# Optimization experiments

Measured on AMD Instinct MI355X. Metric: run time of the kernel, lower is better.

Reference implementation:

```python
import jax, jax.numpy as jnp
import numpy as np

DEPTH = 13                 # tree depth -> N = 2**DEPTH - 1 reaches (heap layout, outlet = node 0)
N = 2 ** DEPTH - 1         # 8191 reaches
T = 2048                   # timesteps


def setup_inputs() -> dict:
    key = jax.random.key(0)
    ks = jax.random.split(key, 8)
    u = lambda k, shape, lo, hi: jax.random.uniform(k, shape, minval=lo, maxval=hi, dtype=jnp.float32)
    return {
        "lateral_inflows": u(ks[0], (T, N), 0.0, 2.0),     # m^3/s lateral inflow per reach
        "manning_n":       u(ks[1], (N,), 0.025, 0.06),    # Manning roughness
        "lengths":         u(ks[2], (N,), 1000.0, 5000.0), # reach length [m]
        "slopes":          u(ks[3], (N,), 1e-4, 1e-2),     # bed slope (>= 1e-4 as in source)
        "width_coefs":     u(ks[4], (N,), 3.0, 10.0),      # w = wc * Q**we  (power-law geometry)
        "width_exps":      u(ks[5], (N,), 0.4, 0.6),
        "depth_coefs":     u(ks[6], (N,), 0.2, 0.5),       # h = dc * Q**de
        "depth_exps":      u(ks[7], (N,), 0.3, 0.45),
        "dt": 3600,                                        # routing timestep [s]
    }


def _mc_outflow(I_new, I_old, O_old, n, L, S, wc, we, dc, de, dt):
    """Variable-parameter Muskingum-Cunge update for one vector of reaches."""
    Qr = jnp.maximum(0.5 * (I_new + O_old), 1e-3)          # reference discharge
    h = dc * Qr ** de                                       # hydraulic depth
    w = wc * Qr ** we                                       # top width
    v = h ** (2.0 / 3.0) * jnp.sqrt(S) / n                  # Manning velocity
    c = jnp.maximum((5.0 / 3.0) * v, 1e-3)                  # kinematic celerity
    K = L / c                                               # travel time
    X = jnp.clip(0.5 * (1.0 - Qr / (w * S * c * L)), 0.0, 0.5)
    den = 2.0 * K * (1.0 - X) + dt
    C1 = (dt - 2.0 * K * X) / den
    C2 = (dt + 2.0 * K * X) / den
    C3 = (2.0 * K * (1.0 - X) - dt) / den
    return jnp.maximum(C1 * I_new + C2 * I_old + C3 * O_old, 0.0)


def reference(lateral_inflows, manning_n, lengths, slopes, width_coefs, width_exps,
              depth_coefs, depth_exps, dt):
    dtf = jnp.float32(dt)
    Np = lateral_inflows.shape[1]
    params = (manning_n, lengths, slopes, width_coefs, width_exps, depth_coefs, depth_exps)

    def step(carry, lat_t):
        I_old, O_old = carry                                # [N] prev inflow / outflow
        Q = jnp.zeros(Np, dtype=lat_t.dtype)                # new outflows this timestep
        I_all = jnp.zeros(Np, dtype=lat_t.dtype)
        # process levels leaves -> root (reverse topological order over the DAG)
        for l in range(DEPTH - 1, -1, -1):
            s, e = 2 ** l - 1, 2 ** (l + 1) - 1             # nodes of level l
            if l == DEPTH - 1:
                up = jnp.float32(0.0)                        # headwater reaches
            else:
                cs, ce = 2 ** (l + 1) - 1, 2 ** (l + 2) - 1  # children = level l+1
                up = Q[cs:ce:2] + Q[cs + 1:ce:2]             # sum of 2 upstream discharges
            I_new = lat_t[s:e] + up
            O_new = _mc_outflow(I_new, I_old[s:e], O_old[s:e],
                                *(p[s:e] for p in params), dtf)
            Q = Q.at[s:e].set(O_new)
            I_all = I_all.at[s:e].set(I_new)
        return (I_all, Q), Q[0]                              # outlet = root (index 0)

    init = (jnp.zeros(Np, jnp.float32), jnp.zeros(Np, jnp.float32))
    _, outlet_Q = jax.lax.scan(step, init, lateral_inflows)
    return outlet_Q                                          # [T]
```

## Files before the change

### kernel.cpp

```cpp
#include <hip/hip_runtime.h>


#define NN 8191
#define TT 2048
#define FBATCH 32
#define NBLK 39
#define BTHREADS 256

#define FLAGS_FOFF 16773120ull
#define REQ_BYTES  67106816ull
#define FLAG_STRIDE 16

#if __has_builtin(__builtin_amdgcn_exp2f)
__device__ __forceinline__ float fexp2(float x) { return __builtin_amdgcn_exp2f(x); }
#else
__device__ __forceinline__ float fexp2(float x) { return exp2f(x); }
#endif
#if __has_builtin(__builtin_amdgcn_logf)
__device__ __forceinline__ float flog2(float x) { return __builtin_amdgcn_logf(x); }
#else
__device__ __forceinline__ float flog2(float x) { return log2f(x); }
#endif
#if __has_builtin(__builtin_amdgcn_rcpf)
__device__ __forceinline__ float frcp(float x) { return __builtin_amdgcn_rcpf(x); }
#else
__device__ __forceinline__ float frcp(float x) { return 1.0f / x; }
#endif

__constant__ int g_level[NBLK] = {
    12,12,12,12,12,12,12,12,12,12,12,12,12,12,12,12,
    11,11,11,11,11,11,11,11,
    10,10,10,10,
    9,9,
    8,7,6,5,4,3,2,1,0};
__constant__ int g_cnt[NBLK] = {
    256,256,256,256,256,256,256,256,256,256,256,256,256,256,256,256,
    256,256,256,256,256,256,256,256,
    256,256,256,256,
    256,256,
    256,128,64,32,16,8,4,2,1};
__constant__ int g_first[13] = {38,37,36,35,34,33,32,31,30,28,24,16,0};
__constant__ unsigned long long g_off[13] = {
    16773120ull, 16769024ull, 16760832ull, 16744448ull, 16711680ull,
    16646144ull, 16515072ull, 16252928ull, 15728640ull, 14680064ull,
    12582912ull, 8388608ull, 0ull};

__device__ __forceinline__ void waitflags(const unsigned int* fa, const unsigned int* fb,
                                          unsigned int target)
{
    while (true) {
        unsigned int a = __hip_atomic_load(fa, __ATOMIC_RELAXED, __HIP_MEMORY_SCOPE_AGENT);
        unsigned int b = fb ? __hip_atomic_load(fb, __ATOMIC_RELAXED, __HIP_MEMORY_SCOPE_AGENT)
                            : a;
        if (a >= target && b >= target) break;
        __builtin_amdgcn_s_sleep(1);
    }
    __builtin_amdgcn_sched_barrier(0);
    asm volatile("" ::: "memory");
}

__global__ void zero_flags(unsigned int* flags)
{
    for (int i = threadIdx.x; i < NBLK * 4 * FLAG_STRIDE; i += 256) flags[i] = 0;
}

__global__ __launch_bounds__(BTHREADS, 1)
void pipe_kernel(const float* __restrict__ lat,
                 const float* __restrict__ nman,
                 const float* __restrict__ len,
                 const float* __restrict__ slp,
                 const float* __restrict__ wcf,
                 const float* __restrict__ wex,
                 const float* __restrict__ dcf,
                 const float* __restrict__ dex,
                 const int*   __restrict__ dtp,
                 float*       __restrict__ out,
                 float*       __restrict__ ws)
{
    const int bid = blockIdx.x;
    const int tid = threadIdx.x;
    const int lvl = g_level[bid];
    const int cnt = g_cnt[bid];
    const int W   = tid >> 6;
    const int wn  = cnt - W * 64;
    if (wn <= 0) return;

    const bool active = (tid < cnt);
    const int B = bid - g_first[lvl];
    const int m = B * 256 + (active ? tid : 0);
    const int node = ((1 << lvl) - 1) + m;
    const int wbase = B * 256 + W * 64;

    unsigned int* flags = (unsigned int*)(ws + FLAGS_FOFF);
    unsigned int* myflag = flags + ((size_t)bid * 4 + W) * FLAG_STRIDE;

    const bool haschild = (lvl < 12);
    const unsigned int* fa = nullptr;
    const unsigned int* fb = nullptr;
    if (haschild) {
        const int Fp = g_first[lvl + 1];
        const int nw = wn < 64 ? wn : 64;
        const int p0 = (2 * wbase) >> 6;
        const int p1 = (2 * wbase + 2 * nw - 1) >> 6;
        fa = flags + ((size_t)(Fp + (p0 >> 2)) * 4 + (p0 & 3)) * FLAG_STRIDE;
        fb = (p1 != p0)
           ? flags + ((size_t)(Fp + (p1 >> 2)) * 4 + (p1 & 3)) * FLAG_STRIDE
           : nullptr;
    }

    const int myW = 1 << lvl;
    const int childW = 1 << (lvl + 1);
    float* myBuf = ws + g_off[lvl];
    const unsigned long long* childBuf =
        haschild ? (const unsigned long long*)(ws + g_off[lvl + 1]) : nullptr;

    const float dtf = (float)dtp[0];

    float em, tkc, ex, k1;
    float Iold = 0.0f, Oold = 0.0f;
    {
        float n = nman[node], L = len[node], S = slp[node];
        float wc = wcf[node], we = wex[node], dc = dcf[node], de = dex[node];
        float dc23 = fexp2(0.6666667f * flog2(dc));
        float cc = 1.6666667f * dc23 * sqrtf(S) * frcp(n);
        float e23 = 0.6666667f * de;
        em  = -e23;
        tkc = 2.0f * L * frcp(cc);
        ex  = 1.0f - we - e23;
        k1  = 0.5f * frcp(S * L * wc * cc);
    }

    float la[FBATCH], c0[FBATCH], c1[FBATCH];

    for (int t0 = 0; t0 < TT; t0 += FBATCH) {
        if (haschild) waitflags(fa, fb, (unsigned int)(t0 + FBATCH));

        if (active) {
#pragma unroll
            for (int k = 0; k < FBATCH; ++k)
                la[k] = lat[(size_t)(t0 + k) * NN + node];
            if (haschild) {
#pragma unroll
                for (int k = 0; k < FBATCH; ++k) {
                    unsigned long long cv = __hip_atomic_load(
                        childBuf + ((size_t)(t0 + k) * childW >> 1) + m,
                        __ATOMIC_RELAXED, __HIP_MEMORY_SCOPE_AGENT);
                    float2 c = *(float2*)&cv;
                    c0[k] = c.x; c1[k] = c.y;
                }
            }
        }
        __builtin_amdgcn_sched_barrier(0);

        if (active) {
#pragma unroll
            for (int k = 0; k < FBATCH; ++k) {
                float Inew = la[k] + (haschild ? (c0[k] + c1[k]) : 0.0f);
                float Qr = fmaxf(0.5f * (Inew + Oold), 1e-3f);
                float lg = flog2(Qr);
                float twoK = tkc * fexp2(em * lg);
                float X = fmaxf(0.5f - k1 * fexp2(ex * lg), 0.0f);
                float A = twoK * X;
                float Bv = twoK - A;
                float r = frcp(Bv + dtf);
                float num = dtf * (Inew + Iold - Oold) + A * (Iold - Inew) + Bv * Oold;
                float O = fmaxf(num * r, 0.0f);
                Iold = Inew; Oold = O;
                if (lvl > 0)
                    __hip_atomic_store(myBuf + (size_t)(t0 + k) * myW + m, O,
                                       __ATOMIC_RELAXED, __HIP_MEMORY_SCOPE_AGENT);
                else
                    out[t0 + k] = O;
            }
        }

        if (lvl > 0) {
            asm volatile("s_waitcnt vmcnt(0)" ::: "memory");
            if ((tid & 63) == 0)
                __hip_atomic_store(myflag, (unsigned int)(t0 + FBATCH),
                                   __ATOMIC_RELAXED, __HIP_MEMORY_SCOPE_AGENT);
        }
    }
}

#define NTHREADS 1024
__device__ __forceinline__ float mc_update_fb(float Inew, float Iold, float Oold,
                                              float em, float tkc, float ex, float k1,
                                              float dtf)
{
    float Qr = fmaxf(0.5f * (Inew + Oold), 1e-3f);
    float lg = flog2(Qr);
    float twoK = tkc * fexp2(em * lg);
    float X = fmaxf(0.5f - k1 * fexp2(ex * lg), 0.0f);
    float A = twoK * X;
    float B = twoK - A;
    float r = frcp(B + dtf);
    float C1 = (dtf - A) * r;
    float C2 = (dtf + A) * r;
    float C3 = (B - dtf) * r;
    return fmaxf(C1 * Inew + C2 * Iold + C3 * Oold, 0.0f);
}

__global__ __launch_bounds__(NTHREADS)
void route_kernel(const float* __restrict__ lat,
                  const float* __restrict__ nman,
                  const float* __restrict__ len,
                  const float* __restrict__ slp,
                  const float* __restrict__ wcf,
                  const float* __restrict__ wex,
                  const float* __restrict__ dcf,
                  const float* __restrict__ dex,
                  const int*   __restrict__ dtp,
                  float*       __restrict__ out)
{
    __shared__ float Osh[NN];
    const int tid = threadIdx.x;
    const float dtf = (float)dtp[0];

    int nodes[8];
    nodes[0] = 4095 + tid;
    nodes[1] = 5119 + tid;
    nodes[2] = 6143 + tid;
    nodes[3] = 7167 + tid;
    nodes[4] = 2047 + tid;
    nodes[5] = 3071 + tid;
    nodes[6] = 1023 + tid;
    nodes[7] = (tid < 1023) ? tid : 0;

    float em[8], tkc[8], ex[8], k1[8];
    float Ireg[8], Oreg[8];
#pragma unroll
    for (int k = 0; k < 8; ++k) {
        int i = nodes[k];
        float n = nman[i], L = len[i], S = slp[i];
        float wc = wcf[i], we = wex[i], dc = dcf[i], de = dex[i];
        float dc23 = fexp2(0.6666667f * flog2(dc));
        float cc = 1.6666667f * dc23 * sqrtf(S) * frcp(n);
        float e23 = 0.6666667f * de;
        em[k]  = -e23;
        tkc[k] = 2.0f * L * frcp(cc);
        ex[k]  = 1.0f - we - e23;
        k1[k]  = 0.5f * frcp(S * L * wc * cc);
        Ireg[k] = 0.0f; Oreg[k] = 0.0f;
    }
    for (int i = tid; i < NN; i += NTHREADS) Osh[i] = 0.0f;
    __syncthreads();

    for (int t = 0; t < TT; ++t) {
        const float* __restrict__ latt = lat + (size_t)t * NN;
#pragma unroll
        for (int k = 0; k < 4; ++k) {
            int i = nodes[k];
            float Inew = latt[i];
            float O = mc_update_fb(Inew, Ireg[k], Oreg[k], em[k], tkc[k], ex[k], k1[k], dtf);
            Ireg[k] = Inew; Oreg[k] = O; Osh[i] = O;
        }
        __syncthreads();
#pragma unroll
        for (int k = 4; k < 6; ++k) {
            int i = nodes[k];
            float Inew = latt[i] + Osh[2 * i + 1] + Osh[2 * i + 2];
            float O = mc_update_fb(Inew, Ireg[k], Oreg[k], em[k], tkc[k], ex[k], k1[k], dtf);
            Ireg[k] = Inew; Oreg[k] = O; Osh[i] = O;
        }
        __syncthreads();
        {
            int i = nodes[6];
            float Inew = latt[i] + Osh[2 * i + 1] + Osh[2 * i + 2];
            float O = mc_update_fb(Inew, Ireg[6], Oreg[6], em[6], tkc[6], ex[6], k1[6], dtf);
            Ireg[6] = Inew; Oreg[6] = O; Osh[i] = O;
        }
        __syncthreads();
        for (int l = 9; l >= 0; --l) {
            int s = (1 << l) - 1;
            int e = (1 << (l + 1)) - 1;
            if (tid >= s && tid < e) {
                int i = tid;
                float Inew = latt[i] + Osh[2 * i + 1] + Osh[2 * i + 2];
                float O = mc_update_fb(Inew, Ireg[7], Oreg[7], em[7], tkc[7], ex[7], k1[7], dtf);
                Ireg[7] = Inew; Oreg[7] = O; Osh[i] = O;
            }
            __syncthreads();
        }
        if (tid == 0) out[t] = Oreg[7];
    }
}

extern "C" void kernel_launch(void* const* d_in, const int* in_sizes, int n_in,
                              void* d_out, int out_size, void* d_ws, size_t ws_size,
                              hipStream_t stream) {
    const float* lat  = (const float*)d_in[0];
    const float* nman = (const float*)d_in[1];
    const float* len  = (const float*)d_in[2];
    const float* slp  = (const float*)d_in[3];
    const float* wcf  = (const float*)d_in[4];
    const float* wex  = (const float*)d_in[5];
    const float* dcf  = (const float*)d_in[6];
    const float* dex  = (const float*)d_in[7];
    const int*   dtp  = (const int*)d_in[8];
    float* out = (float*)d_out;

    if (ws_size >= REQ_BYTES) {
        float* ws = (float*)d_ws;
        unsigned int* flags = (unsigned int*)(ws + FLAGS_FOFF);
        zero_flags<<<dim3(1), dim3(256), 0, stream>>>(flags);
        pipe_kernel<<<dim3(NBLK), dim3(BTHREADS), 0, stream>>>(
            lat, nman, len, slp, wcf, wex, dcf, dex, dtp, out, ws);
    } else {
        route_kernel<<<dim3(1), dim3(NTHREADS), 0, stream>>>(
            lat, nman, len, slp, wcf, wex, dcf, dex, dtp, out);
    }
}
```

Measured before the change: 455.9 us.

## Double-buffer lateral and child loads to prefetch next batch during compute

The per-batch load-then-compute loop becomes a two-stage software pipeline with A/B register buffers. Lateral inflows and child outflows for the next batch are issued with inline-asm global loads, the child loads bypassing cache via sc0 sc1, while the current batch's serial Muskingum-Cunge chain runs. This aims to hide global memory latency behind the dependent transcendental chain. In exchange, each level must wait for its children's flag one batch ahead before computing the current batch, which adds inter-level pipeline skew and roughly doubles register use for the buffers.

```diff
diff --git a/kernel.cpp b/kernel.cpp
--- a/kernel.cpp
+++ b/kernel.cpp
@@ -130,57 +130,89 @@
         k1  = 0.5f * frcp(S * L * wc * cc);
     }
 
-    float la[FBATCH], c0[FBATCH], c1[FBATCH];
-
-    for (int t0 = 0; t0 < TT; t0 += FBATCH) {
-        if (haschild) waitflags(fa, fb, (unsigned int)(t0 + FBATCH));
-
-        if (active) {
-#pragma unroll
-            for (int k = 0; k < FBATCH; ++k)
-                la[k] = lat[(size_t)(t0 + k) * NN + node];
-            if (haschild) {
-#pragma unroll
-                for (int k = 0; k < FBATCH; ++k) {
-                    unsigned long long cv = __hip_atomic_load(
-                        childBuf + ((size_t)(t0 + k) * childW >> 1) + m,
-                        __ATOMIC_RELAXED, __HIP_MEMORY_SCOPE_AGENT);
-                    float2 c = *(float2*)&cv;
-                    c0[k] = c.x; c1[k] = c.y;
-                }
-            }
-        }
-        __builtin_amdgcn_sched_barrier(0);
-
-        if (active) {
-#pragma unroll
-            for (int k = 0; k < FBATCH; ++k) {
-                float Inew = la[k] + (haschild ? (c0[k] + c1[k]) : 0.0f);
-                float Qr = fmaxf(0.5f * (Inew + Oold), 1e-3f);
-                float lg = flog2(Qr);
-                float twoK = tkc * fexp2(em * lg);
-                float X = fmaxf(0.5f - k1 * fexp2(ex * lg), 0.0f);
-                float A = twoK * X;
-                float Bv = twoK - A;
-                float r = frcp(Bv + dtf);
-                float num = dtf * (Inew + Iold - Oold) + A * (Iold - Inew) + Bv * Oold;
-                float O = fmaxf(num * r, 0.0f);
-                Iold = Inew; Oold = O;
-                if (lvl > 0)
-                    __hip_atomic_store(myBuf + (size_t)(t0 + k) * myW + m, O,
-                                       __ATOMIC_RELAXED, __HIP_MEMORY_SCOPE_AGENT);
-                else
-                    out[t0 + k] = O;
-            }
-        }
-
-        if (lvl > 0) {
-            asm volatile("s_waitcnt vmcnt(0)" ::: "memory");
-            if ((tid & 63) == 0)
-                __hip_atomic_store(myflag, (unsigned int)(t0 + FBATCH),
-                                   __ATOMIC_RELAXED, __HIP_MEMORY_SCOPE_AGENT);
-        }
-    }
+    float laA[FBATCH], laB[FBATCH];
+    unsigned long long cvA[FBATCH], cvB[FBATCH];
+
+#define LATBURST(dst, tb)                                                      \
+    if (active) {                                                              \
+        _Pragma("unroll")                                                      \
+        for (int k = 0; k < FBATCH; ++k) {                                     \
+            const float* lp_ = lat + (size_t)((tb) + k) * NN + node;           \
+            asm volatile("global_load_dword %0, %1, off"                       \
+                         : "=v"(dst[k]) : "v"(lp_));                           \
+        }                                                                      \
+    }
+
+#define CHILDBURST(dst, tb)                                                    \
+    if (haschild && active) {                                                  \
+        _Pragma("unroll")                                                      \
+        for (int k = 0; k < FBATCH; ++k) {                                     \
+            const unsigned long long* cp_ =                                    \
+                childBuf + (((size_t)((tb) + k) * childW) >> 1) + m;           \
+            asm volatile("global_load_dwordx2 %0, %1, off sc0 sc1"             \
+                         : "=v"(dst[k]) : "v"(cp_));                           \
+        }                                                                      \
+    }
+
+#define CHAIN(laC, cvC, tb)                                                    \
+    if (active) {                                                              \
+        _Pragma("unroll")                                                      \
+        for (int k = 0; k < FBATCH; ++k) {                                     \
+            float ch_ = 0.0f;                                                  \
+            if (haschild) {                                                    \
+                float c0_ = __uint_as_float((unsigned int)(cvC[k] & 0xffffffffull)); \
+                float c1_ = __uint_as_float((unsigned int)(cvC[k] >> 32));     \
+                ch_ = c0_ + c1_;                                               \
+            }                                                                  \
+            float Inew = laC[k] + ch_;                                         \
+            float Qr = fmaxf(0.5f * (Inew + Oold), 1e-3f);                     \
+            float lg = flog2(Qr);                                              \
+            float twoK = tkc * fexp2(em * lg);                                 \
+            float X = fmaxf(0.5f - k1 * fexp2(ex * lg), 0.0f);                 \
+            float A = twoK * X;                                                \
+            float Bv = twoK - A;                                               \
+            float r = frcp(Bv + dtf);                                          \
+            float num = dtf * (Inew + Iold - Oold) + A * (Iold - Inew) + Bv * Oold; \
+            float O = fmaxf(num * r, 0.0f);                                    \
+            Iold = Inew; Oold = O;                                             \
+            if (lvl > 0)                                                       \
+                __hip_atomic_store(myBuf + (size_t)((tb) + k) * myW + m, O,    \
+                                   __ATOMIC_RELAXED, __HIP_MEMORY_SCOPE_AGENT);\
+            else                                                               \
+                out[(tb) + k] = O;                                             \
+        }                                                                      \
+    }
+
+#define PHASE(laC, cvC, laN, cvN, T0)                                          \
+    do {                                                                       \
+        const int t1_ = (T0) + FBATCH;                                         \
+        if (t1_ < TT) {                                                        \
+            LATBURST(laN, t1_);                                                \
+            if (haschild) waitflags(fa, fb, (unsigned int)(t1_ + FBATCH));     \
+            CHILDBURST(cvN, t1_);                                              \
+        }                                                                      \
+        CHAIN(laC, cvC, (T0));                                                 \
+        asm volatile("s_waitcnt vmcnt(0)" ::: "memory");                       \
+        __builtin_amdgcn_sched_barrier(0);                                     \
+        if (lvl > 0 && (tid & 63) == 0)                                        \
+            __hip_atomic_store(myflag, (unsigned int)((T0) + FBATCH),          \
+                               __ATOMIC_RELAXED, __HIP_MEMORY_SCOPE_AGENT);    \
+    } while (0)
+
+    LATBURST(laA, 0);
+    if (haschild) waitflags(fa, fb, (unsigned int)FBATCH);
+    CHILDBURST(cvA, 0);
+    asm volatile("s_waitcnt vmcnt(0)" ::: "memory");
+    __builtin_amdgcn_sched_barrier(0);
+
+    for (int t0 = 0; t0 < TT; t0 += 2 * FBATCH) {
+        PHASE(laA, cvA, laB, cvB, t0);
+        PHASE(laB, cvB, laA, cvA, t0 + FBATCH);
+    }
+#undef LATBURST
+#undef CHILDBURST
+#undef CHAIN
+#undef PHASE
 }
 
 #define NTHREADS 1024
```

After: 455.6 us. About the same (-0.1%).
